# Kernel optimization log

Hardware: AMD Instinct MI355X
Metric: run time of the kernel (lower is better)

The kernel has to match this reference:

```python
import jax, jax.numpy as jnp
import numpy as np

TEMPERATURE = 8.0  # sqrt(d_k=64)
MASK_FILL = -1e10  # -10000000000.0 in the original


def setup_inputs() -> dict:
    key = jax.random.key(0)
    kq, kk, kv, ke, km = jax.random.split(key, 5)
    B, Lq, Lk, D = 16, 2048, 2048, 64
    q = jax.random.normal(kq, (B, Lq, D), dtype=jnp.float32)
    k = jax.random.normal(kk, (B, Lk, D), dtype=jnp.float32)
    v = jax.random.normal(kv, (B, Lk, D), dtype=jnp.float32)
    explain_weight = jax.random.uniform(ke, (B, Lq, Lk), dtype=jnp.float32)
    mask = jax.random.randint(km, (B, Lq, Lk), 0, 2).astype(bool)
    return {"q": q, "k": k, "v": v, "explain_weight": explain_weight, "mask": mask}


def reference(q, k, v, explain_weight, mask):
    # attn = bmm(q, k^T) / temperature, masked fill, softmax over keys
    attn = jnp.einsum("bqd,bkd->bqk", q, k) / TEMPERATURE
    attn = jnp.where(mask, MASK_FILL, attn)
    attn = jax.nn.softmax(attn, axis=2)
    # dropout is identity in eval mode; post-softmax explain reweighting
    attn = attn * explain_weight
    output = jnp.einsum("bqk,bkd->bqd", attn, v)
    return (output, attn)
```

## Files before the change

kernel.cpp:

```cpp
#include <hip/hip_runtime.h>
#include <cstdint>
#include <cstddef>

#define NB 16
#define NL 2048
#define ND 64
#define QT 16
#define NW 8
#define NTHREADS (NW * 64)
#define SLICE (NL / NW)
#define NT (SLICE / 16)
#define ROWU 1026
#define ELSU (QT * ROWU)
#define LDSB (ELSU * 4)

typedef __attribute__((ext_vector_type(8))) short bf16x8;
typedef __attribute__((ext_vector_type(4))) float f32x4;
typedef __attribute__((ext_vector_type(4))) int i32x4;
typedef __attribute__((ext_vector_type(4))) unsigned short u16x4;
typedef __attribute__((ext_vector_type(2))) unsigned int u32x2;
typedef __attribute__((ext_vector_type(4))) unsigned int u32x4;
typedef unsigned short u16;

#define MFMA __builtin_amdgcn_mfma_f32_16x16x32_bf16

__device__ __forceinline__ u16 f2bf(float x) {
  union { float f; uint32_t u; } v; v.f = x;
  uint32_t r = v.u + 0x7FFFu + ((v.u >> 16) & 1u);
  return (u16)(r >> 16);
}
__device__ __forceinline__ float bfhi2f(uint32_t w) {
  union { uint32_t u; float f; } v; v.u = w & 0xFFFF0000u; return v.f;
}
__device__ __forceinline__ float bflo2f(uint32_t w) {
  union { uint32_t u; float f; } v; v.u = w << 16; return v.f;
}
__device__ __forceinline__ int swzb(int cb) { return cb ^ (((cb >> 7) & 7) << 4); }

template <int MODE>
__device__ __forceinline__ uint32_t mnib(const void* __restrict__ m, size_t i) {
  if constexpr (MODE == 1) {
    const uint32_t x = __builtin_nontemporal_load((const uint32_t*)((const uint8_t*)m + i));
    return (x | (x >> 7) | (x >> 14) | (x >> 21)) & 0xFu;
  } else if constexpr (MODE == 0) {
    const i32x4 x = __builtin_nontemporal_load(((const i32x4*)((const int*)m + i)));
    return (uint32_t)(x[0] != 0) | ((uint32_t)(x[1] != 0) << 1) |
           ((uint32_t)(x[2] != 0) << 2) | ((uint32_t)(x[3] != 0) << 3);
  } else if constexpr (MODE == 2) {
    const f32x4 x = __builtin_nontemporal_load(((const f32x4*)((const float*)m + i)));
    return (uint32_t)(x[0] != 0.f) | ((uint32_t)(x[1] != 0.f) << 1) |
           ((uint32_t)(x[2] != 0.f) << 2) | ((uint32_t)(x[3] != 0.f) << 3);
  } else {
    const uint32_t* p = (const uint32_t*)m + 2 * i;
    return (uint32_t)(p[0] != 0u) | ((uint32_t)(p[2] != 0u) << 1) |
           ((uint32_t)(p[4] != 0u) << 2) | ((uint32_t)(p[6] != 0u) << 3);
  }
}

template <bool WS>
__device__ __forceinline__ void loadKfrag(const float* __restrict__ k,
                                          const u16* __restrict__ kb,
                                          int b, int row, int kg,
                                          bf16x8& b0, bf16x8& b1) {
  if constexpr (WS) {
    const u16* kp = kb + ((size_t)(b * NL + row)) * ND + kg * 8;
    b0 = *(const bf16x8*)kp;
    b1 = *(const bf16x8*)(kp + 32);
  } else {
    const float* kp = k + ((size_t)(b * NL + row)) * ND + kg * 8;
#pragma unroll
    for (int i = 0; i < 8; ++i) {
      b0[i] = (short)f2bf(kp[i]);
      b1[i] = (short)f2bf(kp[i + 32]);
    }
  }
}

template <int MMODE, bool WS>
__device__ __forceinline__ void attn_core(
    const float* __restrict__ q, const float* __restrict__ k,
    const float* __restrict__ v, const float* __restrict__ ew,
    const void* __restrict__ mask,
    const u16* __restrict__ qs, const u16* __restrict__ kb,
    const u16* __restrict__ vt, const uint32_t* __restrict__ mb,
    float* __restrict__ out, float* __restrict__ attn,
    uint32_t* __restrict__ els, float* __restrict__ rsums) {
  const int tid = threadIdx.x;
  const int lane = tid & 63;
  const int w = tid >> 6;
  const int fr = lane & 15;
  const int kg = lane >> 4;

  const int bid = blockIdx.x;
  const int swzid = (bid & 7) * ((NB * (NL / QT)) / 8) + (bid >> 3);
  const int b = swzid >> 7;
  const int q0 = (swzid & 127) * QT;
  const int cbase = w * SLICE;
  const size_t bq = (size_t)b * NL + q0;
  const size_t lrow = bq * NL + (size_t)fr * NL + (size_t)(cbase + 4 * kg);

  bf16x8 a0, a1;
  if constexpr (WS) {
    const u16* qp = qs + (bq + fr) * ND + kg * 8;
    a0 = *(const bf16x8*)qp;
    a1 = *(const bf16x8*)(qp + 32);
  } else {
    const float* qp = q + (bq + fr) * ND + kg * 8;
#pragma unroll
    for (int i = 0; i < 8; ++i) {
      a0[i] = (short)f2bf(qp[i] * 0.125f);
      a1[i] = (short)f2bf(qp[i + 32] * 0.125f);
    }
  }

  uint32_t mw[8];
  if constexpr (WS) {
    const uint32_t* mbr = mb + (bq + fr) * (NL / 32) + (cbase >> 5);
#pragma unroll
    for (int u = 0; u < 8; ++u) mw[u] = mbr[u];
  }

  float rs = 0.f;
#pragma unroll
  for (int ti = 0; ti < NT; ++ti) {
    const int c0 = cbase + ti * 16;
    bf16x8 b0, b1;
    loadKfrag<WS>(k, kb, b, c0 + fr, kg, b0, b1);
    f32x4 s = {0.f, 0.f, 0.f, 0.f};
    s = MFMA(b0, a0, s, 0, 0, 0);
    s = MFMA(b1, a1, s, 0, 0, 0);
    uint32_t nib;
    if constexpr (WS) nib = (mw[ti >> 1] >> (16 * (ti & 1) + 4 * kg)) & 0xFu;
    else              nib = mnib<MMODE>(mask, lrow + (size_t)(ti * 16));
    const float e0 = (nib & 1u) ? 0.f : __expf(s[0]);
    const float e1 = (nib & 2u) ? 0.f : __expf(s[1]);
    const float e2 = (nib & 4u) ? 0.f : __expf(s[2]);
    const float e3 = (nib & 8u) ? 0.f : __expf(s[3]);
    rs += (e0 + e1) + (e2 + e3);
    u32x2 ep;
    ep[0] = (uint32_t)f2bf(e0) | ((uint32_t)f2bf(e1) << 16);
    ep[1] = (uint32_t)f2bf(e2) | ((uint32_t)f2bf(e3) << 16);
    *(u32x2*)(els + fr * ROWU + (swzb((c0 + 4 * kg) * 2) >> 2)) = ep;
  }

  const float* ewbase = ew + bq * NL + cbase + 4 * lane;
  f32x4 ewr[16];
#pragma unroll
  for (int r = 0; r < 16; ++r)
    ewr[r] = __builtin_nontemporal_load((const f32x4*)(ewbase + (size_t)r * NL));
  __builtin_amdgcn_sched_barrier(0);

  rs += __shfl_xor(rs, 16, 64);
  rs += __shfl_xor(rs, 32, 64);
  if (lane < 16) rsums[w * QT + fr] = rs;
  __syncthreads();

  float invf = 0.f;
#pragma unroll
  for (int ww = 0; ww < NW; ++ww) invf += rsums[ww * QT + fr];
  invf = 1.0f / invf;

  float* atb = attn + bq * NL + cbase + 4 * lane;
  const int lofs = swzb((cbase + 4 * lane) * 2) >> 2;
#pragma unroll
  for (int r = 0; r < 16; ++r) {
    const u32x2 el = *(const u32x2*)(els + r * ROWU + lofs);
    const float inv_r = __shfl(invf, r, 64);
    f32x4 p;
    p[0] = bflo2f(el[0]) * inv_r * ewr[r][0];
    p[1] = bfhi2f(el[0]) * inv_r * ewr[r][1];
    p[2] = bflo2f(el[1]) * inv_r * ewr[r][2];
    p[3] = bfhi2f(el[1]) * inv_r * ewr[r][3];
    __builtin_nontemporal_store(p, (f32x4*)(atb + (size_t)r * NL));
    u32x2 pp;
    pp[0] = (uint32_t)f2bf(p[0]) | ((uint32_t)f2bf(p[1]) << 16);
    pp[1] = (uint32_t)f2bf(p[2]) | ((uint32_t)f2bf(p[3]) << 16);
    *(u32x2*)(els + r * ROWU + lofs) = pp;
  }

  f32x4 oA[4] = {{0.f,0.f,0.f,0.f},{0.f,0.f,0.f,0.f},{0.f,0.f,0.f,0.f},{0.f,0.f,0.f,0.f}};
#pragma unroll
  for (int gi = 0; gi < NT / 2; ++gi) {
    union { u32x4 u; bf16x8 v8; } pu;
    pu.u = *(const u32x4*)(els + fr * ROWU + (swzb((cbase + 32 * gi + 8 * kg) * 2) >> 2));
    const bf16x8 pa = pu.v8;
    const int kk = cbase + gi * 32 + kg * 8;
    if constexpr (WS) {
      const u16* vp = vt + ((size_t)(b * ND + fr)) * NL + kk;
      oA[0] = MFMA(pa, *(const bf16x8*)(vp),           oA[0], 0, 0, 0);
      oA[1] = MFMA(pa, *(const bf16x8*)(vp + 16 * NL), oA[1], 0, 0, 0);
      oA[2] = MFMA(pa, *(const bf16x8*)(vp + 32 * NL), oA[2], 0, 0, 0);
      oA[3] = MFMA(pa, *(const bf16x8*)(vp + 48 * NL), oA[3], 0, 0, 0);
    } else {
#pragma unroll
      for (int dt = 0; dt < 4; ++dt) {
        bf16x8 vf;
#pragma unroll
        for (int i = 0; i < 8; ++i)
          vf[i] = (short)f2bf(v[((size_t)(b * NL + kk + i)) * ND + dt * 16 + fr]);
        oA[dt] = MFMA(pa, vf, oA[dt], 0, 0, 0);
      }
    }
  }
  __syncthreads();

  float* osta = (float*)els;
  f32x4 acc = {0.f, 0.f, 0.f, 0.f};
  const int rrr = tid >> 4;
  const int d4 = (tid & 15) * 4;
#pragma unroll
  for (int round = 0; round < NW / 2; ++round) {
    if ((w >> 1) == round) {
      float* od = osta + (w & 1) * (QT * ND);
#pragma unroll
      for (int dt = 0; dt < 4; ++dt)
#pragma unroll
        for (int j = 0; j < 4; ++j)
          od[(4 * kg + j) * ND + dt * 16 + fr] = oA[dt][j];
    }
    __syncthreads();
    if (tid < QT * ND / 4) {
      acc += *(const f32x4*)(osta + rrr * ND + d4) +
             *(const f32x4*)(osta + QT * ND + rrr * ND + d4);
    }
    __syncthreads();
  }
  if (tid < QT * ND / 4)
    *(f32x4*)(out + (bq + rrr) * ND + d4) = acc;
}

__global__ void __launch_bounds__(NTHREADS, 4)
attn_ws(const float* __restrict__ q, const float* __restrict__ k,
        const float* __restrict__ v, const float* __restrict__ ew,
        const u16* __restrict__ qs, const u16* __restrict__ kb,
        const u16* __restrict__ vt, const uint32_t* __restrict__ mb,
        float* __restrict__ out, float* __restrict__ attn) {
  extern __shared__ uint32_t els[];
  __shared__ float rsums[NW * QT];
  attn_core<0, true>(q, k, v, ew, nullptr, qs, kb, vt, mb, out, attn, els, rsums);
}

__global__ void __launch_bounds__(NTHREADS, 4)
attn_fb(const float* __restrict__ q, const float* __restrict__ k,
        const float* __restrict__ v, const float* __restrict__ ew,
        const void* __restrict__ mask,
        float* __restrict__ out, float* __restrict__ attn) {
  extern __shared__ uint32_t els[];
  __shared__ float rsums[NW * QT];
  __shared__ int s_mode;
  if (threadIdx.x < 64) {
    const uint32_t x = ((const uint32_t*)mask)[threadIdx.x];
    const int all01 = __all(x <= 1u);
    const int allf  = __all(x == 0u || x == 0x3F800000u);
    const int oddz  = __all(((threadIdx.x & 1) == 0) || (x == 0u));
    if (threadIdx.x == 0) s_mode = all01 ? (oddz ? 3 : 0) : (allf ? 2 : 1);
  }
  __syncthreads();
  switch (s_mode) {
    case 0:  attn_core<0, false>(q, k, v, ew, mask, nullptr, nullptr, nullptr, nullptr, out, attn, els, rsums); break;
    case 1:  attn_core<1, false>(q, k, v, ew, mask, nullptr, nullptr, nullptr, nullptr, out, attn, els, rsums); break;
    case 2:  attn_core<2, false>(q, k, v, ew, mask, nullptr, nullptr, nullptr, nullptr, out, attn, els, rsums); break;
    default: attn_core<3, false>(q, k, v, ew, mask, nullptr, nullptr, nullptr, nullptr, out, attn, els, rsums); break;
  }
}

__global__ void __launch_bounds__(256)
prep_qk(const float* __restrict__ q, const float* __restrict__ k,
        u16* __restrict__ qs, u16* __restrict__ kb) {
  const size_t NQ4 = (size_t)NB * NL * ND / 4;
  const size_t i = (size_t)blockIdx.x * 256 + threadIdx.x;
  f32x4 val;
  u16* dst;
  if (i < NQ4) {
    val = ((const f32x4*)q)[i];
    val *= 0.125f;
    dst = qs + i * 4;
  } else {
    val = ((const f32x4*)k)[i - NQ4];
    dst = kb + (i - NQ4) * 4;
  }
  u16x4 o;
#pragma unroll
  for (int j = 0; j < 4; ++j) o[j] = f2bf(val[j]);
  *(u16x4*)dst = o;
}

__global__ void __launch_bounds__(256)
prep_vt(const float* __restrict__ v, u16* __restrict__ vt) {
  __shared__ float t[64 * 68];
  const int b = blockIdx.y;
  const int k0 = blockIdx.x * 64;
  const int tid = threadIdx.x;
  const int rr = tid >> 4;
  const int c4 = (tid & 15) * 4;
#pragma unroll
  for (int i = 0; i < 4; ++i) {
    const int r = rr + 16 * i;
    const f32x4 val = *(const f32x4*)(v + ((size_t)(b * NL + k0 + r)) * ND + c4);
    *(f32x4*)(t + r * 68 + c4) = val;
  }
  __syncthreads();
#pragma unroll
  for (int i = 0; i < 4; ++i) {
    const int d = rr + 16 * i;
    u16x4 o;
#pragma unroll
    for (int j = 0; j < 4; ++j) o[j] = f2bf(t[(c4 + j) * 68 + d]);
    *(u16x4*)(vt + ((size_t)(b * ND + d)) * NL + k0 + c4) = o;
  }
}

__global__ void __launch_bounds__(256)
prep_mask(const void* __restrict__ mask, uint32_t* __restrict__ mb) {
  __shared__ int pm;
  if (threadIdx.x < 64) {
    const uint32_t x = ((const uint32_t*)mask)[threadIdx.x];
    const int all01 = __all(x <= 1u);
    const int allf  = __all(x == 0u || x == 0x3F800000u);
    const int oddz  = __all(((threadIdx.x & 1) == 0) || (x == 0u));
    if (threadIdx.x == 0) pm = all01 ? (oddz ? 3 : 0) : (allf ? 2 : 1);
  }
  __syncthreads();
  const int mode = pm;
  const size_t t = (size_t)blockIdx.x * 256 + threadIdx.x;
  uint32_t bits = 0;
  if (mode == 1) {
    const u32x4 x0 = *(((const u32x4*)mask) + t * 2);
    const u32x4 x1 = *(((const u32x4*)mask) + t * 2 + 1);
#pragma unroll
    for (int i = 0; i < 4; ++i)
#pragma unroll
      for (int by = 0; by < 4; ++by) {
        bits |= (((x0[i] >> (8 * by)) & 0xFFu) ? 1u : 0u) << (i * 4 + by);
        bits |= (((x1[i] >> (8 * by)) & 0xFFu) ? 1u : 0u) << (16 + i * 4 + by);
      }
  } else if (mode == 0 || mode == 2) {
#pragma unroll
    for (int c = 0; c < 8; ++c) {
      const u32x4 x = *(((const u32x4*)mask) + t * 8 + c);
#pragma unroll
      for (int i = 0; i < 4; ++i) bits |= (x[i] ? 1u : 0u) << (c * 4 + i);
    }
  } else {
    const uint32_t* p = (const uint32_t*)mask;
#pragma unroll
    for (int i = 0; i < 32; ++i) bits |= (p[2 * (t * 32 + i)] ? 1u : 0u) << i;
  }
  mb[t] = bits;
}

extern "C" void kernel_launch(void* const* d_in, const int* in_sizes, int n_in,
                              void* d_out, int out_size, void* d_ws, size_t ws_size,
                              hipStream_t stream) {
  const float* q    = (const float*)d_in[0];
  const float* k    = (const float*)d_in[1];
  const float* v    = (const float*)d_in[2];
  const float* ew   = (const float*)d_in[3];
  const void*  mask = d_in[4];
  float* out  = (float*)d_out;
  float* attn = out + (size_t)NB * NL * ND;

  const size_t QE = (size_t)NB * NL * ND;
  const size_t MBW = (size_t)NB * NL * (NL / 32);
  u16* qs = (u16*)d_ws;
  u16* kb = qs + QE;
  u16* vt = kb + QE;
  uint32_t* mb = (uint32_t*)(vt + QE);

  (void)hipFuncSetAttribute(reinterpret_cast<const void*>(attn_ws),
                            hipFuncAttributeMaxDynamicSharedMemorySize, LDSB);
  (void)hipFuncSetAttribute(reinterpret_cast<const void*>(attn_fb),
                            hipFuncAttributeMaxDynamicSharedMemorySize, LDSB);

  dim3 grid(NB * (NL / QT));
  if (ws_size >= 3 * QE * sizeof(u16) + MBW * sizeof(uint32_t)) {
    prep_qk<<<dim3((unsigned)(2 * QE / 4 / 256)), 256, 0, stream>>>(q, k, qs, kb);
    prep_vt<<<dim3(NL / 64, NB), 256, 0, stream>>>(v, vt);
    prep_mask<<<dim3((unsigned)(MBW / 256)), 256, 0, stream>>>(mask, mb);
    attn_ws<<<grid, NTHREADS, LDSB, stream>>>(q, k, v, ew, qs, kb, vt, mb, out, attn);
  } else {
    attn_fb<<<grid, NTHREADS, LDSB, stream>>>(q, k, v, ew, mask, out, attn);
  }
}
```

Baseline: 248.0 us.

## Split fused attention into exp-score and PV kernels via bf16 workspace

```diff
diff --git a/kernel.cpp b/kernel.cpp
--- a/kernel.cpp
+++ b/kernel.cpp
@@ -13,6 +13,7 @@
 #define ROWU 1026
 #define ELSU (QT * ROWU)
 #define LDSB (ELSU * 4)
+#define QEC (NB * NL * ND)
 
 typedef __attribute__((ext_vector_type(8))) short bf16x8;
 typedef __attribute__((ext_vector_type(4))) float f32x4;
@@ -74,6 +75,155 @@
       b1[i] = (short)f2bf(kp[i + 32]);
     }
   }
+}
+
+__global__ void __launch_bounds__(NTHREADS, 4)
+attn_e(const u16* __restrict__ qs, const u16* __restrict__ kb,
+       const uint32_t* __restrict__ mb,
+       u16* __restrict__ ews, float* __restrict__ invw) {
+  extern __shared__ uint32_t els[];
+  __shared__ float rsums[NW * QT];
+  const int tid = threadIdx.x;
+  const int lane = tid & 63;
+  const int w = tid >> 6;
+  const int fr = lane & 15;
+  const int kg = lane >> 4;
+
+  const int bid = blockIdx.x;
+  const int swzid = (bid & 7) * ((NB * (NL / QT)) / 8) + (bid >> 3);
+  const int b = swzid >> 7;
+  const int q0 = (swzid & 127) * QT;
+  const int cbase = w * SLICE;
+  const size_t bq = (size_t)b * NL + q0;
+
+  const u16* qp = qs + (bq + fr) * ND + kg * 8;
+  const bf16x8 a0 = *(const bf16x8*)qp;
+  const bf16x8 a1 = *(const bf16x8*)(qp + 32);
+
+  uint32_t mw[8];
+  const uint32_t* mbr = mb + (bq + fr) * (NL / 32) + (cbase >> 5);
+#pragma unroll
+  for (int u = 0; u < 8; ++u) mw[u] = mbr[u];
+
+  float rs = 0.f;
+#pragma unroll
+  for (int ti = 0; ti < NT; ++ti) {
+    const int c0 = cbase + ti * 16;
+    bf16x8 b0, b1;
+    loadKfrag<true>(nullptr, kb, b, c0 + fr, kg, b0, b1);
+    f32x4 s = {0.f, 0.f, 0.f, 0.f};
+    s = MFMA(b0, a0, s, 0, 0, 0);
+    s = MFMA(b1, a1, s, 0, 0, 0);
+    const uint32_t nib = (mw[ti >> 1] >> (16 * (ti & 1) + 4 * kg)) & 0xFu;
+    const float e0 = (nib & 1u) ? 0.f : __expf(s[0]);
+    const float e1 = (nib & 2u) ? 0.f : __expf(s[1]);
+    const float e2 = (nib & 4u) ? 0.f : __expf(s[2]);
+    const float e3 = (nib & 8u) ? 0.f : __expf(s[3]);
+    rs += (e0 + e1) + (e2 + e3);
+    u32x2 ep;
+    ep[0] = (uint32_t)f2bf(e0) | ((uint32_t)f2bf(e1) << 16);
+    ep[1] = (uint32_t)f2bf(e2) | ((uint32_t)f2bf(e3) << 16);
+    *(u32x2*)(els + fr * ROWU + (swzb((c0 + 4 * kg) * 2) >> 2)) = ep;
+  }
+  rs += __shfl_xor(rs, 16, 64);
+  rs += __shfl_xor(rs, 32, 64);
+  if (lane < 16) rsums[w * QT + fr] = rs;
+  __syncthreads();
+
+  float invf = 0.f;
+#pragma unroll
+  for (int ww = 0; ww < NW; ++ww) invf += rsums[ww * QT + fr];
+  invf = 1.0f / invf;
+  if (w == 0 && lane < 16) invw[bq + fr] = invf;
+
+  const int lofs = swzb((cbase + 4 * lane) * 2) >> 2;
+  u16* eb = ews + bq * NL + cbase + 4 * lane;
+#pragma unroll
+  for (int r = 0; r < 16; ++r) {
+    const u32x2 el = *(const u32x2*)(els + r * ROWU + lofs);
+    __builtin_nontemporal_store(el, (u32x2*)(eb + (size_t)r * NL));
+  }
+}
+
+__global__ void __launch_bounds__(NTHREADS, 4)
+attn_spv(const u16* __restrict__ ews, const float* __restrict__ invw,
+         const float* __restrict__ ew, const u16* __restrict__ vt,
+         float* __restrict__ out, float* __restrict__ attn) {
+  extern __shared__ uint32_t els[];
+  const int tid = threadIdx.x;
+  const int lane = tid & 63;
+  const int w = tid >> 6;
+  const int fr = lane & 15;
+  const int kg = lane >> 4;
+
+  const int bid = blockIdx.x;
+  const int swzid = (bid & 7) * ((NB * (NL / QT)) / 8) + (bid >> 3);
+  const int b = swzid >> 7;
+  const int q0 = (swzid & 127) * QT;
+  const int cbase = w * SLICE;
+  const size_t bq = (size_t)b * NL + q0;
+
+  const float invf = invw[bq + fr];
+
+  const int lofs = swzb((cbase + 4 * lane) * 2) >> 2;
+  const u16* eb = ews + bq * NL + cbase + 4 * lane;
+  const float* ewb = ew + bq * NL + cbase + 4 * lane;
+  float* atb = attn + bq * NL + cbase + 4 * lane;
+#pragma unroll
+  for (int r = 0; r < 16; ++r) {
+    const u32x2 el = __builtin_nontemporal_load((const u32x2*)(eb + (size_t)r * NL));
+    const f32x4 w4 = __builtin_nontemporal_load((const f32x4*)(ewb + (size_t)r * NL));
+    const float inv_r = __shfl(invf, r, 64);
+    f32x4 p;
+    p[0] = bflo2f(el[0]) * inv_r * w4[0];
+    p[1] = bfhi2f(el[0]) * inv_r * w4[1];
+    p[2] = bflo2f(el[1]) * inv_r * w4[2];
+    p[3] = bfhi2f(el[1]) * inv_r * w4[3];
+    __builtin_nontemporal_store(p, (f32x4*)(atb + (size_t)r * NL));
+    u32x2 pp;
+    pp[0] = (uint32_t)f2bf(p[0]) | ((uint32_t)f2bf(p[1]) << 16);
+    pp[1] = (uint32_t)f2bf(p[2]) | ((uint32_t)f2bf(p[3]) << 16);
+    *(u32x2*)(els + r * ROWU + lofs) = pp;
+  }
+
+  f32x4 oA[4] = {{0.f,0.f,0.f,0.f},{0.f,0.f,0.f,0.f},{0.f,0.f,0.f,0.f},{0.f,0.f,0.f,0.f}};
+#pragma unroll
+  for (int gi = 0; gi < NT / 2; ++gi) {
+    union { u32x4 u; bf16x8 v8; } pu;
+    pu.u = *(const u32x4*)(els + fr * ROWU + (swzb((cbase + 32 * gi + 8 * kg) * 2) >> 2));
+    const bf16x8 pa = pu.v8;
+    const int kk = cbase + gi * 32 + kg * 8;
+    const u16* vp = vt + ((size_t)(b * ND + fr)) * NL + kk;
+    oA[0] = MFMA(pa, *(const bf16x8*)(vp),           oA[0], 0, 0, 0);
+    oA[1] = MFMA(pa, *(const bf16x8*)(vp + 16 * NL), oA[1], 0, 0, 0);
+    oA[2] = MFMA(pa, *(const bf16x8*)(vp + 32 * NL), oA[2], 0, 0, 0);
+    oA[3] = MFMA(pa, *(const bf16x8*)(vp + 48 * NL), oA[3], 0, 0, 0);
+  }
+  __syncthreads();
+
+  float* osta = (float*)els;
+  f32x4 acc = {0.f, 0.f, 0.f, 0.f};
+  const int rrr = tid >> 4;
+  const int d4 = (tid & 15) * 4;
+#pragma unroll
+  for (int round = 0; round < NW / 2; ++round) {
+    if ((w >> 1) == round) {
+      float* od = osta + (w & 1) * (QT * ND);
+#pragma unroll
+      for (int dt = 0; dt < 4; ++dt)
+#pragma unroll
+        for (int j = 0; j < 4; ++j)
+          od[(4 * kg + j) * ND + dt * 16 + fr] = oA[dt][j];
+    }
+    __syncthreads();
+    if (tid < QT * ND / 4) {
+      acc += *(const f32x4*)(osta + rrr * ND + d4) +
+             *(const f32x4*)(osta + QT * ND + rrr * ND + d4);
+    }
+    __syncthreads();
+  }
+  if (tid < QT * ND / 4)
+    *(f32x4*)(out + (bq + rrr) * ND + d4) = acc;
 }
 
 template <int MMODE, bool WS>
@@ -142,14 +292,6 @@
     ep[1] = (uint32_t)f2bf(e2) | ((uint32_t)f2bf(e3) << 16);
     *(u32x2*)(els + fr * ROWU + (swzb((c0 + 4 * kg) * 2) >> 2)) = ep;
   }
-
-  const float* ewbase = ew + bq * NL + cbase + 4 * lane;
-  f32x4 ewr[16];
-#pragma unroll
-  for (int r = 0; r < 16; ++r)
-    ewr[r] = __builtin_nontemporal_load((const f32x4*)(ewbase + (size_t)r * NL));
-  __builtin_amdgcn_sched_barrier(0);
-
   rs += __shfl_xor(rs, 16, 64);
   rs += __shfl_xor(rs, 32, 64);
   if (lane < 16) rsums[w * QT + fr] = rs;
@@ -161,16 +303,18 @@
   invf = 1.0f / invf;
 
   float* atb = attn + bq * NL + cbase + 4 * lane;
+  const float* ewb = ew + bq * NL + cbase + 4 * lane;
   const int lofs = swzb((cbase + 4 * lane) * 2) >> 2;
 #pragma unroll
   for (int r = 0; r < 16; ++r) {
     const u32x2 el = *(const u32x2*)(els + r * ROWU + lofs);
+    const f32x4 w4 = __builtin_nontemporal_load((const f32x4*)(ewb + (size_t)r * NL));
     const float inv_r = __shfl(invf, r, 64);
     f32x4 p;
-    p[0] = bflo2f(el[0]) * inv_r * ewr[r][0];
-    p[1] = bfhi2f(el[0]) * inv_r * ewr[r][1];
-    p[2] = bflo2f(el[1]) * inv_r * ewr[r][2];
-    p[3] = bfhi2f(el[1]) * inv_r * ewr[r][3];
+    p[0] = bflo2f(el[0]) * inv_r * w4[0];
+    p[1] = bfhi2f(el[0]) * inv_r * w4[1];
+    p[2] = bflo2f(el[1]) * inv_r * w4[2];
+    p[3] = bfhi2f(el[1]) * inv_r * w4[3];
     __builtin_nontemporal_store(p, (f32x4*)(atb + (size_t)r * NL));
     u32x2 pp;
     pp[0] = (uint32_t)f2bf(p[0]) | ((uint32_t)f2bf(p[1]) << 16);
@@ -264,25 +408,65 @@
   }
 }
 
+#define QKB ((unsigned)(2 * QEC / 4 / 256))
 __global__ void __launch_bounds__(256)
-prep_qk(const float* __restrict__ q, const float* __restrict__ k,
-        u16* __restrict__ qs, u16* __restrict__ kb) {
-  const size_t NQ4 = (size_t)NB * NL * ND / 4;
-  const size_t i = (size_t)blockIdx.x * 256 + threadIdx.x;
-  f32x4 val;
-  u16* dst;
-  if (i < NQ4) {
-    val = ((const f32x4*)q)[i];
-    val *= 0.125f;
-    dst = qs + i * 4;
+prep_a(const float* __restrict__ q, const float* __restrict__ k,
+       u16* __restrict__ qs, u16* __restrict__ kb,
+       const void* __restrict__ mask, uint32_t* __restrict__ mb) {
+  if (blockIdx.x < QKB) {
+    const size_t NQ4 = (size_t)QEC / 4;
+    const size_t i = (size_t)blockIdx.x * 256 + threadIdx.x;
+    f32x4 val;
+    u16* dst;
+    if (i < NQ4) {
+      val = ((const f32x4*)q)[i];
+      val *= 0.125f;
+      dst = qs + i * 4;
+    } else {
+      val = ((const f32x4*)k)[i - NQ4];
+      dst = kb + (i - NQ4) * 4;
+    }
+    u16x4 o;
+#pragma unroll
+    for (int j = 0; j < 4; ++j) o[j] = f2bf(val[j]);
+    *(u16x4*)dst = o;
+    return;
+  }
+  __shared__ int pm;
+  if (threadIdx.x < 64) {
+    const uint32_t x = ((const uint32_t*)mask)[threadIdx.x];
+    const int all01 = __all(x <= 1u);
+    const int allf  = __all(x == 0u || x == 0x3F800000u);
+    const int oddz  = __all(((threadIdx.x & 1) == 0) || (x == 0u));
+    if (threadIdx.x == 0) pm = all01 ? (oddz ? 3 : 0) : (allf ? 2 : 1);
+  }
+  __syncthreads();
+  const int mode = pm;
+  const size_t t = (size_t)(blockIdx.x - QKB) * 256 + threadIdx.x;
+  uint32_t bits = 0;
+  if (mode == 1) {
+    const u32x4 x0 = *(((const u32x4*)mask) + t * 2);
+    const u32x4 x1 = *(((const u32x4*)mask) + t * 2 + 1);
+#pragma unroll
+    for (int i = 0; i < 4; ++i)
+#pragma unroll
+      for (int by = 0; by < 4; ++by) {
+        bits |= (((x0[i] >> (8 * by)) & 0xFFu) ? 1u : 0u) << (i * 4 + by);
+        bits |= (((x1[i] >> (8 * by)) & 0xFFu) ? 1u : 0u) << (16 + i * 4 + by);
+      }
+  } else if (mode == 0 || mode == 2) {
+#pragma unroll
+    for (int c = 0; c < 8; ++c) {
+      const u32x4 x = *(((const u32x4*)mask) + t * 8 + c);
+#pragma unroll
+      for (int i = 0; i < 4; ++i) bits |= (x[i] ? 1u : 0u) << (c * 4 + i);
+    }
   } else {
-    val = ((const f32x4*)k)[i - NQ4];
-    dst = kb + (i - NQ4) * 4;
-  }
-  u16x4 o;
-#pragma unroll
-  for (int j = 0; j < 4; ++j) o[j] = f2bf(val[j]);
-  *(u16x4*)dst = o;
+    const uint32_t* p = (const uint32_t*)mask;
+#pragma unroll
+    for (int i = 0; i < 32; ++i) bits |= (p[2 * (t * 32 + i)] ? 1u : 0u) << i;
+  }
+  mb[t] = bits;
 }
 
 __global__ void __launch_bounds__(256)
@@ -308,45 +492,6 @@
     for (int j = 0; j < 4; ++j) o[j] = f2bf(t[(c4 + j) * 68 + d]);
     *(u16x4*)(vt + ((size_t)(b * ND + d)) * NL + k0 + c4) = o;
   }
-}
-
-__global__ void __launch_bounds__(256)
-prep_mask(const void* __restrict__ mask, uint32_t* __restrict__ mb) {
-  __shared__ int pm;
-  if (threadIdx.x < 64) {
-    const uint32_t x = ((const uint32_t*)mask)[threadIdx.x];
-    const int all01 = __all(x <= 1u);
-    const int allf  = __all(x == 0u || x == 0x3F800000u);
-    const int oddz  = __all(((threadIdx.x & 1) == 0) || (x == 0u));
-    if (threadIdx.x == 0) pm = all01 ? (oddz ? 3 : 0) : (allf ? 2 : 1);
-  }
-  __syncthreads();
-  const int mode = pm;
-  const size_t t = (size_t)blockIdx.x * 256 + threadIdx.x;
-  uint32_t bits = 0;
-  if (mode == 1) {
-    const u32x4 x0 = *(((const u32x4*)mask) + t * 2);
-    const u32x4 x1 = *(((const u32x4*)mask) + t * 2 + 1);
-#pragma unroll
-    for (int i = 0; i < 4; ++i)
-#pragma unroll
-      for (int by = 0; by < 4; ++by) {
-        bits |= (((x0[i] >> (8 * by)) & 0xFFu) ? 1u : 0u) << (i * 4 + by);
-        bits |= (((x1[i] >> (8 * by)) & 0xFFu) ? 1u : 0u) << (16 + i * 4 + by);
-      }
-  } else if (mode == 0 || mode == 2) {
-#pragma unroll
-    for (int c = 0; c < 8; ++c) {
-      const u32x4 x = *(((const u32x4*)mask) + t * 8 + c);
-#pragma unroll
-      for (int i = 0; i < 4; ++i) bits |= (x[i] ? 1u : 0u) << (c * 4 + i);
-    }
-  } else {
-    const uint32_t* p = (const uint32_t*)mask;
-#pragma unroll
-    for (int i = 0; i < 32; ++i) bits |= (p[2 * (t * 32 + i)] ? 1u : 0u) << i;
-  }
-  mb[t] = bits;
 }
 
 extern "C" void kernel_launch(void* const* d_in, const int* in_sizes, int n_in,
@@ -360,23 +505,37 @@
   float* out  = (float*)d_out;
   float* attn = out + (size_t)NB * NL * ND;
 
-  const size_t QE = (size_t)NB * NL * ND;
+  const size_t QE = (size_t)QEC;
   const size_t MBW = (size_t)NB * NL * (NL / 32);
   u16* qs = (u16*)d_ws;
   u16* kb = qs + QE;
   u16* vt = kb + QE;
   uint32_t* mb = (uint32_t*)(vt + QE);
-
+  float* invw = (float*)(mb + MBW);
+  u16* ews = (u16*)(invw + (size_t)NB * NL);
+
+  const size_t need_base  = 3 * QE * sizeof(u16) + MBW * sizeof(uint32_t);
+  const size_t need_split = need_base + (size_t)NB * NL * sizeof(float) +
+                            (size_t)NB * NL * NL * sizeof(u16);
+
+  (void)hipFuncSetAttribute(reinterpret_cast<const void*>(attn_e),
+                            hipFuncAttributeMaxDynamicSharedMemorySize, LDSB);
+  (void)hipFuncSetAttribute(reinterpret_cast<const void*>(attn_spv),
+                            hipFuncAttributeMaxDynamicSharedMemorySize, LDSB);
   (void)hipFuncSetAttribute(reinterpret_cast<const void*>(attn_ws),
                             hipFuncAttributeMaxDynamicSharedMemorySize, LDSB);
   (void)hipFuncSetAttribute(reinterpret_cast<const void*>(attn_fb),
                             hipFuncAttributeMaxDynamicSharedMemorySize, LDSB);
 
   dim3 grid(NB * (NL / QT));
-  if (ws_size >= 3 * QE * sizeof(u16) + MBW * sizeof(uint32_t)) {
-    prep_qk<<<dim3((unsigned)(2 * QE / 4 / 256)), 256, 0, stream>>>(q, k, qs, kb);
+  if (ws_size >= need_split) {
+    prep_a<<<dim3(QKB + (unsigned)(MBW / 256)), 256, 0, stream>>>(q, k, qs, kb, mask, mb);
     prep_vt<<<dim3(NL / 64, NB), 256, 0, stream>>>(v, vt);
-    prep_mask<<<dim3((unsigned)(MBW / 256)), 256, 0, stream>>>(mask, mb);
+    attn_e<<<grid, NTHREADS, LDSB, stream>>>(qs, kb, mb, ews, invw);
+    attn_spv<<<grid, NTHREADS, LDSB, stream>>>(ews, invw, ew, vt, out, attn);
+  } else if (ws_size >= need_base) {
+    prep_a<<<dim3(QKB + (unsigned)(MBW / 256)), 256, 0, stream>>>(q, k, qs, kb, mask, mb);
+    prep_vt<<<dim3(NL / 64, NB), 256, 0, stream>>>(v, vt);
     attn_ws<<<grid, NTHREADS, LDSB, stream>>>(q, k, v, ew, qs, kb, vt, mb, out, attn);
   } else {
     attn_fb<<<grid, NTHREADS, LDSB, stream>>>(q, k, v, ew, mask, out, attn);
```

Result: slower. 291.1 us (+17.4%).

## Defer attn stores past the PV matmul and merge Q/K and mask prep kernels

Applied to the files above, without the earlier changes.

```diff
diff --git a/kernel.cpp b/kernel.cpp
--- a/kernel.cpp
+++ b/kernel.cpp
@@ -13,6 +13,7 @@
 #define ROWU 1026
 #define ELSU (QT * ROWU)
 #define LDSB (ELSU * 4)
+#define QEC (NB * NL * ND)
 
 typedef __attribute__((ext_vector_type(8))) short bf16x8;
 typedef __attribute__((ext_vector_type(4))) float f32x4;
@@ -142,14 +143,6 @@
     ep[1] = (uint32_t)f2bf(e2) | ((uint32_t)f2bf(e3) << 16);
     *(u32x2*)(els + fr * ROWU + (swzb((c0 + 4 * kg) * 2) >> 2)) = ep;
   }
-
-  const float* ewbase = ew + bq * NL + cbase + 4 * lane;
-  f32x4 ewr[16];
-#pragma unroll
-  for (int r = 0; r < 16; ++r)
-    ewr[r] = __builtin_nontemporal_load((const f32x4*)(ewbase + (size_t)r * NL));
-  __builtin_amdgcn_sched_barrier(0);
-
   rs += __shfl_xor(rs, 16, 64);
   rs += __shfl_xor(rs, 32, 64);
   if (lane < 16) rsums[w * QT + fr] = rs;
@@ -160,21 +153,18 @@
   for (int ww = 0; ww < NW; ++ww) invf += rsums[ww * QT + fr];
   invf = 1.0f / invf;
 
-  float* atb = attn + bq * NL + cbase + 4 * lane;
+  const float* ewb = ew + bq * NL + cbase + 4 * lane;
   const int lofs = swzb((cbase + 4 * lane) * 2) >> 2;
 #pragma unroll
   for (int r = 0; r < 16; ++r) {
+    const f32x4 w4 = __builtin_nontemporal_load((const f32x4*)(ewb + (size_t)r * NL));
     const u32x2 el = *(const u32x2*)(els + r * ROWU + lofs);
     const float inv_r = __shfl(invf, r, 64);
-    f32x4 p;
-    p[0] = bflo2f(el[0]) * inv_r * ewr[r][0];
-    p[1] = bfhi2f(el[0]) * inv_r * ewr[r][1];
-    p[2] = bflo2f(el[1]) * inv_r * ewr[r][2];
-    p[3] = bfhi2f(el[1]) * inv_r * ewr[r][3];
-    __builtin_nontemporal_store(p, (f32x4*)(atb + (size_t)r * NL));
     u32x2 pp;
-    pp[0] = (uint32_t)f2bf(p[0]) | ((uint32_t)f2bf(p[1]) << 16);
-    pp[1] = (uint32_t)f2bf(p[2]) | ((uint32_t)f2bf(p[3]) << 16);
+    pp[0] = (uint32_t)f2bf(bflo2f(el[0]) * inv_r * w4[0]) |
+            ((uint32_t)f2bf(bfhi2f(el[0]) * inv_r * w4[1]) << 16);
+    pp[1] = (uint32_t)f2bf(bflo2f(el[1]) * inv_r * w4[2]) |
+            ((uint32_t)f2bf(bfhi2f(el[1]) * inv_r * w4[3]) << 16);
     *(u32x2*)(els + r * ROWU + lofs) = pp;
   }
 
@@ -201,6 +191,18 @@
         oA[dt] = MFMA(pa, vf, oA[dt], 0, 0, 0);
       }
     }
+  }
+
+  float* atb = attn + bq * NL + cbase + 4 * lane;
+#pragma unroll
+  for (int r = 0; r < 16; ++r) {
+    const u32x2 pp = *(const u32x2*)(els + r * ROWU + lofs);
+    f32x4 p;
+    p[0] = bflo2f(pp[0]);
+    p[1] = bfhi2f(pp[0]);
+    p[2] = bflo2f(pp[1]);
+    p[3] = bfhi2f(pp[1]);
+    __builtin_nontemporal_store(p, (f32x4*)(atb + (size_t)r * NL));
   }
   __syncthreads();
 
@@ -264,25 +266,65 @@
   }
 }
 
+#define QKB ((unsigned)(2 * QEC / 4 / 256))
 __global__ void __launch_bounds__(256)
-prep_qk(const float* __restrict__ q, const float* __restrict__ k,
-        u16* __restrict__ qs, u16* __restrict__ kb) {
-  const size_t NQ4 = (size_t)NB * NL * ND / 4;
-  const size_t i = (size_t)blockIdx.x * 256 + threadIdx.x;
-  f32x4 val;
-  u16* dst;
-  if (i < NQ4) {
-    val = ((const f32x4*)q)[i];
-    val *= 0.125f;
-    dst = qs + i * 4;
-  } else {
-    val = ((const f32x4*)k)[i - NQ4];
-    dst = kb + (i - NQ4) * 4;
-  }
-  u16x4 o;
-#pragma unroll
-  for (int j = 0; j < 4; ++j) o[j] = f2bf(val[j]);
-  *(u16x4*)dst = o;
+prep_a(const float* __restrict__ q, const float* __restrict__ k,
+       u16* __restrict__ qs, u16* __restrict__ kb,
+       const void* __restrict__ mask, uint32_t* __restrict__ mb) {
+  if (blockIdx.x < QKB) {
+    const size_t NQ4 = (size_t)QEC / 4;
+    const size_t i = (size_t)blockIdx.x * 256 + threadIdx.x;
+    f32x4 val;
+    u16* dst;
+    if (i < NQ4) {
+      val = ((const f32x4*)q)[i];
+      val *= 0.125f;
+      dst = qs + i * 4;
+    } else {
+      val = ((const f32x4*)k)[i - NQ4];
+      dst = kb + (i - NQ4) * 4;
+    }
+    u16x4 o;
+#pragma unroll
+    for (int j = 0; j < 4; ++j) o[j] = f2bf(val[j]);
+    *(u16x4*)dst = o;
+    return;
+  }
+  __shared__ int pm;
+  if (threadIdx.x < 64) {
+    const uint32_t x = ((const uint32_t*)mask)[threadIdx.x];
+    const int all01 = __all(x <= 1u);
+    const int allf  = __all(x == 0u || x == 0x3F800000u);
+    const int oddz  = __all(((threadIdx.x & 1) == 0) || (x == 0u));
+    if (threadIdx.x == 0) pm = all01 ? (oddz ? 3 : 0) : (allf ? 2 : 1);
+  }
+  __syncthreads();
+  const int mode = pm;
+  const size_t t = (size_t)(blockIdx.x - QKB) * 256 + threadIdx.x;
+  uint32_t bits = 0;
+  if (mode == 1) {
+    const u32x4 x0 = *(((const u32x4*)mask) + t * 2);
+    const u32x4 x1 = *(((const u32x4*)mask) + t * 2 + 1);
+#pragma unroll
+    for (int i = 0; i < 4; ++i)
+#pragma unroll
+      for (int by = 0; by < 4; ++by) {
+        bits |= (((x0[i] >> (8 * by)) & 0xFFu) ? 1u : 0u) << (i * 4 + by);
+        bits |= (((x1[i] >> (8 * by)) & 0xFFu) ? 1u : 0u) << (16 + i * 4 + by);
+      }
+  } else if (mode == 0 || mode == 2) {
+#pragma unroll
+    for (int c = 0; c < 8; ++c) {
+      const u32x4 x = *(((const u32x4*)mask) + t * 8 + c);
+#pragma unroll
+      for (int i = 0; i < 4; ++i) bits |= (x[i] ? 1u : 0u) << (c * 4 + i);
+    }
+  } else {
+    const uint32_t* p = (const uint32_t*)mask;
+#pragma unroll
+    for (int i = 0; i < 32; ++i) bits |= (p[2 * (t * 32 + i)] ? 1u : 0u) << i;
+  }
+  mb[t] = bits;
 }
 
 __global__ void __launch_bounds__(256)
@@ -308,45 +350,6 @@
     for (int j = 0; j < 4; ++j) o[j] = f2bf(t[(c4 + j) * 68 + d]);
     *(u16x4*)(vt + ((size_t)(b * ND + d)) * NL + k0 + c4) = o;
   }
-}
-
-__global__ void __launch_bounds__(256)
-prep_mask(const void* __restrict__ mask, uint32_t* __restrict__ mb) {
-  __shared__ int pm;
-  if (threadIdx.x < 64) {
-    const uint32_t x = ((const uint32_t*)mask)[threadIdx.x];
-    const int all01 = __all(x <= 1u);
-    const int allf  = __all(x == 0u || x == 0x3F800000u);
-    const int oddz  = __all(((threadIdx.x & 1) == 0) || (x == 0u));
-    if (threadIdx.x == 0) pm = all01 ? (oddz ? 3 : 0) : (allf ? 2 : 1);
-  }
-  __syncthreads();
-  const int mode = pm;
-  const size_t t = (size_t)blockIdx.x * 256 + threadIdx.x;
-  uint32_t bits = 0;
-  if (mode == 1) {
-    const u32x4 x0 = *(((const u32x4*)mask) + t * 2);
-    const u32x4 x1 = *(((const u32x4*)mask) + t * 2 + 1);
-#pragma unroll
-    for (int i = 0; i < 4; ++i)
-#pragma unroll
-      for (int by = 0; by < 4; ++by) {
-        bits |= (((x0[i] >> (8 * by)) & 0xFFu) ? 1u : 0u) << (i * 4 + by);
-        bits |= (((x1[i] >> (8 * by)) & 0xFFu) ? 1u : 0u) << (16 + i * 4 + by);
-      }
-  } else if (mode == 0 || mode == 2) {
-#pragma unroll
-    for (int c = 0; c < 8; ++c) {
-      const u32x4 x = *(((const u32x4*)mask) + t * 8 + c);
-#pragma unroll
-      for (int i = 0; i < 4; ++i) bits |= (x[i] ? 1u : 0u) << (c * 4 + i);
-    }
-  } else {
-    const uint32_t* p = (const uint32_t*)mask;
-#pragma unroll
-    for (int i = 0; i < 32; ++i) bits |= (p[2 * (t * 32 + i)] ? 1u : 0u) << i;
-  }
-  mb[t] = bits;
 }
 
 extern "C" void kernel_launch(void* const* d_in, const int* in_sizes, int n_in,
@@ -360,23 +363,24 @@
   float* out  = (float*)d_out;
   float* attn = out + (size_t)NB * NL * ND;
 
-  const size_t QE = (size_t)NB * NL * ND;
+  const size_t QE = (size_t)QEC;
   const size_t MBW = (size_t)NB * NL * (NL / 32);
   u16* qs = (u16*)d_ws;
   u16* kb = qs + QE;
   u16* vt = kb + QE;
   uint32_t* mb = (uint32_t*)(vt + QE);
 
+  const size_t need_base = 3 * QE * sizeof(u16) + MBW * sizeof(uint32_t);
+
   (void)hipFuncSetAttribute(reinterpret_cast<const void*>(attn_ws),
                             hipFuncAttributeMaxDynamicSharedMemorySize, LDSB);
   (void)hipFuncSetAttribute(reinterpret_cast<const void*>(attn_fb),
                             hipFuncAttributeMaxDynamicSharedMemorySize, LDSB);
 
   dim3 grid(NB * (NL / QT));
-  if (ws_size >= 3 * QE * sizeof(u16) + MBW * sizeof(uint32_t)) {
-    prep_qk<<<dim3((unsigned)(2 * QE / 4 / 256)), 256, 0, stream>>>(q, k, qs, kb);
+  if (ws_size >= need_base) {
+    prep_a<<<dim3(QKB + (unsigned)(MBW / 256)), 256, 0, stream>>>(q, k, qs, kb, mask, mb);
     prep_vt<<<dim3(NL / 64, NB), 256, 0, stream>>>(v, vt);
-    prep_mask<<<dim3((unsigned)(MBW / 256)), 256, 0, stream>>>(mask, mb);
     attn_ws<<<grid, NTHREADS, LDSB, stream>>>(q, k, v, ew, qs, kb, vt, mb, out, attn);
   } else {
     attn_fb<<<grid, NTHREADS, LDSB, stream>>>(q, k, v, ew, mask, out, attn);
```

After: 241.0 us. -2.8%, faster.
